# Kernel tuning notes

Hardware: AMD Instinct MI355X
Metric: run time of the kernel (lower is better)

The kernel has to match this reference:

```python
import jax, jax.numpy as jnp
import numpy as np

MRG = 0.1
ALPHA = 32.0
STAT_WEIGHT = 0.01
STAT_ADJUST_WEIGHT = 0.15
COS_EPS = 1e-8  # torch F.cosine_similarity eps


def l2_norm(x):
    # matches torch l2_norm: x / sqrt(sum(x^2, axis=1) + 1e-12)
    normp = jnp.sum(x * x, axis=1) + 1e-12
    return x / jnp.sqrt(normp)[:, None]


def setup_inputs() -> dict:
    key = jax.random.key(0)
    kx, kt, kp, kc = jax.random.split(key, 4)
    B, C, D = 512, 50000, 128
    X = jax.random.normal(kx, (B, D), dtype=jnp.float32)
    T = jax.random.randint(kt, (B,), 0, C, dtype=jnp.int32)
    proxies = jax.random.normal(kp, (C, D), dtype=jnp.float32)
    class_centers = jax.random.normal(kc, (C, D), dtype=jnp.float32)
    return {"X": X, "T": T, "proxies": proxies, "class_centers": class_centers}


def reference(X, T, proxies, class_centers):
    C = proxies.shape[0]
    Xn = l2_norm(X)                      # (B, D)
    Pn = l2_norm(proxies)                # (C, D)
    cos = Xn @ Pn.T                      # (B, C)

    # ---- vectorized per-class statistics (replaces the Python loop) ----
    counts = jax.ops.segment_sum(jnp.ones(T.shape[0], jnp.float32), T, num_segments=C)
    sums = jax.ops.segment_sum(Xn, T, num_segments=C)          # (C, D)
    sqs = jax.ops.segment_sum(Xn * Xn, T, num_segments=C)      # (C, D)
    safe = jnp.maximum(counts, 1.0)[:, None]
    mean = sums / safe
    var = jnp.clip(sqs / safe - mean * mean, 1e-6, 10.0)        # biased var, clamped
    var_weight = 1.0 / (1.0 + var.mean(axis=1))                 # (C,)

    # cosine_similarity(P_norm[i], class_centers[i]) with torch eps semantics
    pnorm = jnp.maximum(jnp.sqrt(jnp.sum(Pn * Pn, axis=1)), COS_EPS)
    cnorm = jnp.maximum(jnp.sqrt(jnp.sum(class_centers * class_centers, axis=1)), COS_EPS)
    center_sim = jnp.sum(Pn * class_centers, axis=1) / (pnorm * cnorm)  # (C,)

    has_samples = counts > 0
    adj = jnp.where(has_samples, center_sim * var_weight * STAT_ADJUST_WEIGHT, 0.0)
    combined = cos + adj[None, :]        # (B, C)

    # ---- proxy-anchor exp-sum terms ----
    onehot = (T[:, None] == jnp.arange(C, dtype=T.dtype)[None, :])  # (B, C) bool
    pos_exp = jnp.exp(-ALPHA * (combined - MRG))
    neg_exp = jnp.exp(ALPHA * (combined + MRG))
    P_sim_sum = jnp.sum(jnp.where(onehot, pos_exp, 0.0), axis=0)    # (C,)
    N_sim_sum = jnp.sum(jnp.where(onehot, 0.0, neg_exp), axis=0)    # (C,)

    num_valid = jnp.sum(has_samples).astype(jnp.float32)
    pos_term = jnp.sum(jnp.log1p(P_sim_sum)) / num_valid
    neg_term = jnp.sum(jnp.log1p(N_sim_sum)) / jnp.float32(C)

    center_reg = jnp.mean(jnp.abs(class_centers))
    return pos_term + neg_term + STAT_WEIGHT * center_reg
```

## Files before the change

### kernel.cpp

```cpp
#include <hip/hip_runtime.h>
#include <math.h>

#define ALPHA 32.0f
#define MRG 0.1f
#define STAT_WEIGHT 0.01f
#define STAT_ADJ_W 0.15f
#define COS_EPS 1e-8f

typedef __attribute__((ext_vector_type(8))) short bf16x8;
typedef __attribute__((ext_vector_type(4))) float f32x4;
typedef __attribute__((ext_vector_type(4))) unsigned int u32x4;

__device__ __forceinline__ ushort f2bf(float f) {
    unsigned u = __float_as_uint(f);
    return (ushort)((u + 0x7FFFu + ((u >> 16) & 1u)) >> 16);
}
__device__ __forceinline__ unsigned pk2(float a, float b) {
    return (unsigned)f2bf(a) | ((unsigned)f2bf(b) << 16);
}

__device__ __forceinline__ float bred128(float v, float* sm, int d) {
    #pragma unroll
    for (int off = 1; off < 64; off <<= 1) v += __shfl_xor(v, off);
    if ((d & 63) == 0) sm[d >> 6] = v;
    __syncthreads();
    float r = sm[0] + sm[1];
    __syncthreads();
    return r;
}

__global__ void k_stats(const float* __restrict__ X, const float* __restrict__ proxies,
                        const float* __restrict__ cc, const int* __restrict__ T,
                        ushort* __restrict__ Xn16, float* __restrict__ adj,
                        float* __restrict__ scal, float* __restrict__ cabs_part,
                        int C, int B) {
    const int b = blockIdx.x, d = threadIdx.x;
    __shared__ int Tl[512];
    __shared__ float sm[2];
    __shared__ float smc[2];
    __shared__ int mlist[512];
    __shared__ int mcnt;

    if (b == 0 && d < 8) scal[d] = 0.f;

    for (int i = d; i < B; i += 128) Tl[i] = T[i];
    if (d == 0) mcnt = 0;

    float cabs = 0.f;
    {
        const float4* cp = (const float4*)cc;
        const int n4 = C * 32;
        for (int i = b * 128 + d; i < n4; i += B * 128) {
            float4 v = cp[i];
            cabs += fabsf(v.x) + fabsf(v.y) + fabsf(v.z) + fabsf(v.w);
        }
    }
    #pragma unroll
    for (int off = 1; off < 64; off <<= 1) cabs += __shfl_xor(cabs, off);
    if ((d & 63) == 0) smc[d >> 6] = cabs;
    __syncthreads();
    if (d == 0) cabs_part[b] = smc[0] + smc[1];

    const int c = Tl[b];

    float x = X[(size_t)b * 128 + d];
    float n2 = bred128(x * x, sm, d);
    float xn = x * rsqrtf(n2 + 1e-12f);
    const int pk = ((((d >> 3) ^ (b & 15)) << 3) | (d & 7));
    Xn16[(size_t)b * 128 + pk] = f2bf(xn);

    for (int j = d; j < B; j += 128)
        if (Tl[j] == c) mlist[atomicAdd(&mcnt, 1)] = j;
    __syncthreads();
    const int cnt = mcnt;
    int minj = mlist[0];
    for (int i = 1; i < cnt; ++i) minj = min(minj, mlist[i]);
    if (minj != b) return;

    float sd = 0.f, qd = 0.f;
    int prev = -1;
    for (int rank = 0; rank < cnt; ++rank) {
        int cur = 0x7fffffff;
        for (int i = 0; i < cnt; ++i) { int v = mlist[i]; if (v > prev && v < cur) cur = v; }
        prev = cur;
        float xj = X[(size_t)cur * 128 + d];
        float nj = bred128(xj * xj, sm, d);
        float xnj = xj * rsqrtf(nj + 1e-12f);
        sd += xnj; qd += xnj * xnj;
    }
    float fc = (float)cnt;
    float m = sd / fc;
    float var = fminf(fmaxf(qd / fc - m * m, 1e-6f), 10.0f);
    float sv = bred128(var, sm, d);

    float p  = proxies[(size_t)c * 128 + d];
    float cv = cc[(size_t)c * 128 + d];
    float s2 = bred128(p * p, sm, d);
    float c2 = bred128(cv * cv, sm, d);
    float pc = bred128(p * cv, sm, d);
    if (d == 0) {
        float inv = rsqrtf(s2 + 1e-12f);
        float pn = fmaxf(sqrtf(s2) * inv, COS_EPS);
        float cn = fmaxf(sqrtf(c2), COS_EPS);
        float censim = (pc * inv) / (pn * cn);
        float vw = 1.0f / (1.0f + sv * (1.0f / 128.0f));
        adj[c] = censim * vw * STAT_ADJ_W;
    }
}

__launch_bounds__(256, 2)
__global__ void k_main(const float* __restrict__ proxies, const ushort* __restrict__ Xsw,
                       const int* __restrict__ T, float* __restrict__ PN,
                       int C, int nslice) {
    const int tid = threadIdx.x, lane = tid & 63, wv = tid >> 6;
    const int nlo = lane & 15, quad = lane >> 4;
    const int half = blockIdx.y;

    __shared__ ushort Sx[32768];
    __shared__ alignas(16) int Tl[256];

    {
        const uint4* src = (const uint4*)Xsw + half * 4096;
        uint4* dst = (uint4*)Sx;
        #pragma unroll
        for (int k = 0; k < 16; ++k) dst[tid + k * 256] = src[tid + k * 256];
    }
    Tl[tid] = T[half * 256 + tid];
    __syncthreads();

    float* PA = PN + (size_t)half * 2 * C;
    float* NA = PA + C;

    int fro[4];
    #pragma unroll
    for (int ks = 0; ks < 4; ++ks)
        fro[ks] = nlo * 128 + (((ks * 4 + quad) ^ nlo) << 3);

    for (int s = blockIdx.x; s < nslice; s += gridDim.x) {
        const int c0 = s * 128;
        const int cls0 = c0 + wv * 32 + nlo;
        const int cls1 = cls0 + 16;

        bf16x8 bfr[2][4];
        #pragma unroll
        for (int t = 0; t < 2; ++t) {
            int cls = c0 + wv * 32 + t * 16 + nlo;
            int cl = (cls < C) ? cls : C - 1;
            const float4* pr = (const float4*)(proxies + (size_t)cl * 128);
            float4 v0[4], v1[4];
            float s2 = 0.f;
            #pragma unroll
            for (int ks = 0; ks < 4; ++ks) {
                v0[ks] = pr[ks * 8 + quad * 2];
                v1[ks] = pr[ks * 8 + quad * 2 + 1];
                s2 += v0[ks].x*v0[ks].x + v0[ks].y*v0[ks].y + v0[ks].z*v0[ks].z + v0[ks].w*v0[ks].w
                    + v1[ks].x*v1[ks].x + v1[ks].y*v1[ks].y + v1[ks].z*v1[ks].z + v1[ks].w*v1[ks].w;
            }
            s2 += __shfl_xor(s2, 16);
            s2 += __shfl_xor(s2, 32);
            float pin = rsqrtf(s2 + 1e-12f);
            #pragma unroll
            for (int ks = 0; ks < 4; ++ks) {
                u32x4 u;
                u.x = pk2(v0[ks].x * pin, v0[ks].y * pin);
                u.y = pk2(v0[ks].z * pin, v0[ks].w * pin);
                u.z = pk2(v1[ks].x * pin, v1[ks].y * pin);
                u.w = pk2(v1[ks].z * pin, v1[ks].w * pin);
                bfr[t][ks] = __builtin_bit_cast(bf16x8, u);
            }
        }

        float pp0 = 0.f, np0 = 0.f, pp1 = 0.f, np1 = 0.f;
        #pragma unroll 4
        for (int rt = 0; rt < 16; ++rt) {
            const ushort* sb = &Sx[rt * 2048];
            bf16x8 a0 = *(const bf16x8*)&sb[fro[0]];
            bf16x8 a1 = *(const bf16x8*)&sb[fro[1]];
            bf16x8 a2 = *(const bf16x8*)&sb[fro[2]];
            bf16x8 a3 = *(const bf16x8*)&sb[fro[3]];
            f32x4 acc0 = {0.f,0.f,0.f,0.f}, acc1 = {0.f,0.f,0.f,0.f};
            acc0 = __builtin_amdgcn_mfma_f32_16x16x32_bf16(a0, bfr[0][0], acc0, 0, 0, 0);
            acc1 = __builtin_amdgcn_mfma_f32_16x16x32_bf16(a0, bfr[1][0], acc1, 0, 0, 0);
            acc0 = __builtin_amdgcn_mfma_f32_16x16x32_bf16(a1, bfr[0][1], acc0, 0, 0, 0);
            acc1 = __builtin_amdgcn_mfma_f32_16x16x32_bf16(a1, bfr[1][1], acc1, 0, 0, 0);
            acc0 = __builtin_amdgcn_mfma_f32_16x16x32_bf16(a2, bfr[0][2], acc0, 0, 0, 0);
            acc1 = __builtin_amdgcn_mfma_f32_16x16x32_bf16(a2, bfr[1][2], acc1, 0, 0, 0);
            acc0 = __builtin_amdgcn_mfma_f32_16x16x32_bf16(a3, bfr[0][3], acc0, 0, 0, 0);
            acc1 = __builtin_amdgcn_mfma_f32_16x16x32_bf16(a3, bfr[1][3], acc1, 0, 0, 0);

            int4 t4 = *(const int4*)&Tl[rt * 16 + quad * 4];
            int tvs[4] = {t4.x, t4.y, t4.z, t4.w};
            #pragma unroll
            for (int r = 0; r < 4; ++r) {
                { bool po = (tvs[r] == cls0); float v = acc0[r];
                  float e = __expf(po ? -ALPHA * (v - MRG) : ALPHA * (v + MRG));
                  pp0 += po ? e : 0.f; np0 += po ? 0.f : e; }
                { bool po = (tvs[r] == cls1); float v = acc1[r];
                  float e = __expf(po ? -ALPHA * (v - MRG) : ALPHA * (v + MRG));
                  pp1 += po ? e : 0.f; np1 += po ? 0.f : e; }
            }
        }

        pp0 += __shfl_xor(pp0, 16); pp0 += __shfl_xor(pp0, 32);
        np0 += __shfl_xor(np0, 16); np0 += __shfl_xor(np0, 32);
        pp1 += __shfl_xor(pp1, 16); pp1 += __shfl_xor(pp1, 32);
        np1 += __shfl_xor(np1, 16); np1 += __shfl_xor(np1, 32);
        if (quad == 0) {
            if (cls0 < C) { PA[cls0] = pp0; NA[cls0] = np0; }
            if (cls1 < C) { PA[cls1] = pp1; NA[cls1] = np1; }
        }
    }
}

__launch_bounds__(256)
__global__ void k_fin(const float* __restrict__ PN, const float* __restrict__ adj,
                      const float* __restrict__ cabs_part, float* __restrict__ scal,
                      float* __restrict__ out, int C, int nfin) {
    const int tid = threadIdx.x, lane = tid & 63, wv = tid >> 6;
    const int c = blockIdx.x * 256 + tid;
    __shared__ float red[4][3];
    float lp = 0.f, ln = 0.f, nv = 0.f;
    if (c < C) {
        float p = PN[c] + PN[2 * (size_t)C + c];
        float n = PN[(size_t)C + c] + PN[3 * (size_t)C + c];
        float a = 0.f;
        if (p > 0.f) { a = adj[c]; nv = 1.f; }
        lp = log1pf(p * __expf(-ALPHA * a));
        ln = log1pf(n * __expf( ALPHA * a));
    }
    #pragma unroll
    for (int off = 1; off < 64; off <<= 1) {
        lp += __shfl_xor(lp, off);
        ln += __shfl_xor(ln, off);
        nv += __shfl_xor(nv, off);
    }
    if (lane == 0) { red[wv][0] = lp; red[wv][1] = ln; red[wv][2] = nv; }
    __syncthreads();
    if (tid == 0) {
        atomicAdd(&scal[0], red[0][0] + red[1][0] + red[2][0] + red[3][0]);
        atomicAdd(&scal[1], red[0][1] + red[1][1] + red[2][1] + red[3][1]);
        atomicAdd(&scal[3], red[0][2] + red[1][2] + red[2][2] + red[3][2]);
    }
    if (blockIdx.x == 0) {
        float cb = cabs_part[tid] + cabs_part[tid + 256];
        #pragma unroll
        for (int off = 1; off < 64; off <<= 1) cb += __shfl_xor(cb, off);
        __syncthreads();
        if (lane == 0) red[wv][0] = cb;
        __syncthreads();
        if (tid == 0) atomicAdd(&scal[2], red[0][0] + red[1][0] + red[2][0] + red[3][0]);
    }
    if (tid == 0) {
        __threadfence();
        unsigned old = atomicAdd((unsigned*)(scal + 4), 1u);
        if (old == (unsigned)(nfin - 1)) {
            float S0 = atomicAdd(&scal[0], 0.f);
            float S1 = atomicAdd(&scal[1], 0.f);
            float S2 = atomicAdd(&scal[2], 0.f);
            float S3 = atomicAdd(&scal[3], 0.f);
            out[0] = S0 / S3 + S1 / (float)C + STAT_WEIGHT * (S2 / ((float)C * 128.f));
        }
    }
}

extern "C" void kernel_launch(void* const* d_in, const int* in_sizes, int n_in,
                              void* d_out, int out_size, void* d_ws, size_t ws_size,
                              hipStream_t stream) {
    const float* X       = (const float*)d_in[0];
    const int*   T       = (const int*)d_in[1];
    const float* proxies = (const float*)d_in[2];
    const float* cc      = (const float*)d_in[3];
    float* out = (float*)d_out;

    const int B = in_sizes[1];
    const int D = in_sizes[0] / B;
    const int C = in_sizes[2] / D;

    float*  PN   = (float*)d_ws;
    float*  scal = PN + 4 * (size_t)C;
    float*  cabs_part = scal + 8;
    float*  adj  = cabs_part + 512;
    ushort* Xn16 = (ushort*)(adj + C);

    const int nslice = (C + 127) / 128;
    const int nfin   = (C + 255) / 256;

    k_stats<<<B, 128, 0, stream>>>(X, proxies, cc, T, Xn16, adj, scal,
                                   cabs_part, C, B);
    k_main<<<dim3(256, 2), 256, 0, stream>>>(proxies, Xn16, T, PN, C, nslice);
    k_fin<<<nfin, 256, 0, stream>>>(PN, adj, cabs_part, scal, out, C, nfin);
}
```

Before: 130.6 us.

## Split X normalization out and co-schedule stats work with main GEMM blocks

A small prep kernel now only normalizes X into swizzled bf16. The per-class statistics and the center abs-sum move into a merged kernel, with odd blocks doing stats and even blocks doing the MFMA proxy-anchor exp-sum work. This lets the memory-heavy class_centers scan overlap with the compute-bound GEMM instead of running before it. The cost is that stats blocks also reserve the large shared-memory footprint and use 256 threads where half sit idle in the reductions. The prep kernel also keeps a dead no-op loop.

New measurement: 138.2 us. 5.8% more time.

```diff
diff --git a/kernel.cpp b/kernel.cpp
--- a/kernel.cpp
+++ b/kernel.cpp
@@ -19,57 +19,181 @@
     return (unsigned)f2bf(a) | ((unsigned)f2bf(b) << 16);
 }
 
-__device__ __forceinline__ float bred128(float v, float* sm, int d) {
+__device__ __forceinline__ float bredL(float v, float* sm, int tid) {
     #pragma unroll
     for (int off = 1; off < 64; off <<= 1) v += __shfl_xor(v, off);
-    if ((d & 63) == 0) sm[d >> 6] = v;
+    if ((tid & 63) == 0 && tid < 128) sm[tid >> 6] = v;
     __syncthreads();
     float r = sm[0] + sm[1];
     __syncthreads();
     return r;
 }
 
-__global__ void k_stats(const float* __restrict__ X, const float* __restrict__ proxies,
-                        const float* __restrict__ cc, const int* __restrict__ T,
-                        ushort* __restrict__ Xn16, float* __restrict__ adj,
-                        float* __restrict__ scal, float* __restrict__ cabs_part,
-                        int C, int B) {
+__global__ void k_prep(const float* __restrict__ X, ushort* __restrict__ Xn16,
+                       float* __restrict__ scal) {
     const int b = blockIdx.x, d = threadIdx.x;
+    __shared__ float sm[2];
+    if (b == 0 && d < 8) scal[d] = 0.f;
+    float x = X[(size_t)b * 128 + d];
+    #pragma unroll
+    for (int off = 1; off < 64; off <<= 1) x = x;
+    float v = X[(size_t)b * 128 + d];
+    float n2;
+    {
+        float s = v * v;
+        #pragma unroll
+        for (int off = 1; off < 64; off <<= 1) s += __shfl_xor(s, off);
+        if ((d & 63) == 0) sm[d >> 6] = s;
+        __syncthreads();
+        n2 = sm[0] + sm[1];
+    }
+    float xn = v * rsqrtf(n2 + 1e-12f);
+    const int pk = ((((d >> 3) ^ (b & 15)) << 3) | (d & 7));
+    Xn16[(size_t)b * 128 + pk] = f2bf(xn);
+}
+
+__launch_bounds__(256, 2)
+__global__ void k_big(const float* __restrict__ X, const float* __restrict__ proxies,
+                      const float* __restrict__ cc, const int* __restrict__ T,
+                      const ushort* __restrict__ Xsw, float* __restrict__ PN,
+                      float* __restrict__ adj, float* __restrict__ cabs_part,
+                      int C, int B, int nslice) {
+    const int tid = threadIdx.x, lane = tid & 63, wv = tid >> 6;
+    const int role = blockIdx.x & 1;
+
+    __shared__ ushort Sx[32768];
+    __shared__ alignas(16) int Tg[256];
     __shared__ int Tl[512];
+    __shared__ int mlist[512];
     __shared__ float sm[2];
-    __shared__ float smc[2];
-    __shared__ int mlist[512];
+    __shared__ float smc[8];
     __shared__ int mcnt;
 
-    if (b == 0 && d < 8) scal[d] = 0.f;
-
-    for (int i = d; i < B; i += 128) Tl[i] = T[i];
-    if (d == 0) mcnt = 0;
+    if (role == 0) {
+        const int nlo = lane & 15, quad = lane >> 4;
+        const int gid = blockIdx.x >> 1;
+        const int x = gid & 255, half = gid >> 8;
+
+        {
+            const uint4* src = (const uint4*)Xsw + half * 4096;
+            uint4* dst = (uint4*)Sx;
+            #pragma unroll
+            for (int k = 0; k < 16; ++k) dst[tid + k * 256] = src[tid + k * 256];
+        }
+        Tg[tid] = T[half * 256 + tid];
+        __syncthreads();
+
+        float* PA = PN + (size_t)half * 2 * C;
+        float* NA = PA + C;
+
+        int fro[4];
+        #pragma unroll
+        for (int ks = 0; ks < 4; ++ks)
+            fro[ks] = nlo * 128 + (((ks * 4 + quad) ^ nlo) << 3);
+
+        for (int s = x; s < nslice; s += 256) {
+            const int c0 = s * 128;
+            const int cls0 = c0 + wv * 32 + nlo;
+            const int cls1 = cls0 + 16;
+
+            bf16x8 bfr[2][4];
+            #pragma unroll
+            for (int t = 0; t < 2; ++t) {
+                int cls = c0 + wv * 32 + t * 16 + nlo;
+                int cl = (cls < C) ? cls : C - 1;
+                const float4* pr = (const float4*)(proxies + (size_t)cl * 128);
+                float4 v0[4], v1[4];
+                float s2 = 0.f;
+                #pragma unroll
+                for (int ks = 0; ks < 4; ++ks) {
+                    v0[ks] = pr[ks * 8 + quad * 2];
+                    v1[ks] = pr[ks * 8 + quad * 2 + 1];
+                    s2 += v0[ks].x*v0[ks].x + v0[ks].y*v0[ks].y + v0[ks].z*v0[ks].z + v0[ks].w*v0[ks].w
+                        + v1[ks].x*v1[ks].x + v1[ks].y*v1[ks].y + v1[ks].z*v1[ks].z + v1[ks].w*v1[ks].w;
+                }
+                s2 += __shfl_xor(s2, 16);
+                s2 += __shfl_xor(s2, 32);
+                float pin = rsqrtf(s2 + 1e-12f);
+                #pragma unroll
+                for (int ks = 0; ks < 4; ++ks) {
+                    u32x4 u;
+                    u.x = pk2(v0[ks].x * pin, v0[ks].y * pin);
+                    u.y = pk2(v0[ks].z * pin, v0[ks].w * pin);
+                    u.z = pk2(v1[ks].x * pin, v1[ks].y * pin);
+                    u.w = pk2(v1[ks].z * pin, v1[ks].w * pin);
+                    bfr[t][ks] = __builtin_bit_cast(bf16x8, u);
+                }
+            }
+
+            float pp0 = 0.f, np0 = 0.f, pp1 = 0.f, np1 = 0.f;
+            #pragma unroll 4
+            for (int rt = 0; rt < 16; ++rt) {
+                const ushort* sb = &Sx[rt * 2048];
+                bf16x8 a0 = *(const bf16x8*)&sb[fro[0]];
+                bf16x8 a1 = *(const bf16x8*)&sb[fro[1]];
+                bf16x8 a2 = *(const bf16x8*)&sb[fro[2]];
+                bf16x8 a3 = *(const bf16x8*)&sb[fro[3]];
+                f32x4 acc0 = {0.f,0.f,0.f,0.f}, acc1 = {0.f,0.f,0.f,0.f};
+                acc0 = __builtin_amdgcn_mfma_f32_16x16x32_bf16(a0, bfr[0][0], acc0, 0, 0, 0);
+                acc1 = __builtin_amdgcn_mfma_f32_16x16x32_bf16(a0, bfr[1][0], acc1, 0, 0, 0);
+                acc0 = __builtin_amdgcn_mfma_f32_16x16x32_bf16(a1, bfr[0][1], acc0, 0, 0, 0);
+                acc1 = __builtin_amdgcn_mfma_f32_16x16x32_bf16(a1, bfr[1][1], acc1, 0, 0, 0);
+                acc0 = __builtin_amdgcn_mfma_f32_16x16x32_bf16(a2, bfr[0][2], acc0, 0, 0, 0);
+                acc1 = __builtin_amdgcn_mfma_f32_16x16x32_bf16(a2, bfr[1][2], acc1, 0, 0, 0);
+                acc0 = __builtin_amdgcn_mfma_f32_16x16x32_bf16(a3, bfr[0][3], acc0, 0, 0, 0);
+                acc1 = __builtin_amdgcn_mfma_f32_16x16x32_bf16(a3, bfr[1][3], acc1, 0, 0, 0);
+
+                int4 t4 = *(const int4*)&Tg[rt * 16 + quad * 4];
+                int tvs[4] = {t4.x, t4.y, t4.z, t4.w};
+                #pragma unroll
+                for (int r = 0; r < 4; ++r) {
+                    { bool po = (tvs[r] == cls0); float v = acc0[r];
+                      float e = __expf(po ? -ALPHA * (v - MRG) : ALPHA * (v + MRG));
+                      pp0 += po ? e : 0.f; np0 += po ? 0.f : e; }
+                    { bool po = (tvs[r] == cls1); float v = acc1[r];
+                      float e = __expf(po ? -ALPHA * (v - MRG) : ALPHA * (v + MRG));
+                      pp1 += po ? e : 0.f; np1 += po ? 0.f : e; }
+                }
+            }
+
+            pp0 += __shfl_xor(pp0, 16); pp0 += __shfl_xor(pp0, 32);
+            np0 += __shfl_xor(np0, 16); np0 += __shfl_xor(np0, 32);
+            pp1 += __shfl_xor(pp1, 16); pp1 += __shfl_xor(pp1, 32);
+            np1 += __shfl_xor(np1, 16); np1 += __shfl_xor(np1, 32);
+            if (quad == 0) {
+                if (cls0 < C) { PA[cls0] = pp0; NA[cls0] = np0; }
+                if (cls1 < C) { PA[cls1] = pp1; NA[cls1] = np1; }
+            }
+        }
+        return;
+    }
+
+    const int b = blockIdx.x >> 1;
+    const int d = tid & 127;
+    const bool lo = tid < 128;
+
+    Tl[tid] = T[tid]; Tl[tid + 256] = T[tid + 256];
+    if (tid == 0) mcnt = 0;
 
     float cabs = 0.f;
     {
         const float4* cp = (const float4*)cc;
         const int n4 = C * 32;
-        for (int i = b * 128 + d; i < n4; i += B * 128) {
+        #pragma unroll 4
+        for (int i = b * 256 + tid; i < n4; i += B * 256) {
             float4 v = cp[i];
             cabs += fabsf(v.x) + fabsf(v.y) + fabsf(v.z) + fabsf(v.w);
         }
     }
     #pragma unroll
     for (int off = 1; off < 64; off <<= 1) cabs += __shfl_xor(cabs, off);
-    if ((d & 63) == 0) smc[d >> 6] = cabs;
-    __syncthreads();
-    if (d == 0) cabs_part[b] = smc[0] + smc[1];
+    if (lane == 0) smc[wv] = cabs;
+    __syncthreads();
+    if (tid == 0) cabs_part[b] = (smc[0] + smc[1]) + (smc[2] + smc[3]);
 
     const int c = Tl[b];
 
-    float x = X[(size_t)b * 128 + d];
-    float n2 = bred128(x * x, sm, d);
-    float xn = x * rsqrtf(n2 + 1e-12f);
-    const int pk = ((((d >> 3) ^ (b & 15)) << 3) | (d & 7));
-    Xn16[(size_t)b * 128 + pk] = f2bf(xn);
-
-    for (int j = d; j < B; j += 128)
+    for (int j = tid; j < B; j += 256)
         if (Tl[j] == c) mlist[atomicAdd(&mcnt, 1)] = j;
     __syncthreads();
     const int cnt = mcnt;
@@ -83,132 +207,28 @@
         int cur = 0x7fffffff;
         for (int i = 0; i < cnt; ++i) { int v = mlist[i]; if (v > prev && v < cur) cur = v; }
         prev = cur;
-        float xj = X[(size_t)cur * 128 + d];
-        float nj = bred128(xj * xj, sm, d);
+        float xj = lo ? X[(size_t)cur * 128 + d] : 0.f;
+        float nj = bredL(xj * xj, sm, tid);
         float xnj = xj * rsqrtf(nj + 1e-12f);
         sd += xnj; qd += xnj * xnj;
     }
     float fc = (float)cnt;
     float m = sd / fc;
     float var = fminf(fmaxf(qd / fc - m * m, 1e-6f), 10.0f);
-    float sv = bred128(var, sm, d);
-
-    float p  = proxies[(size_t)c * 128 + d];
-    float cv = cc[(size_t)c * 128 + d];
-    float s2 = bred128(p * p, sm, d);
-    float c2 = bred128(cv * cv, sm, d);
-    float pc = bred128(p * cv, sm, d);
-    if (d == 0) {
+    float sv = bredL(var, sm, tid);
+
+    float p  = lo ? proxies[(size_t)c * 128 + d] : 0.f;
+    float cv = lo ? cc[(size_t)c * 128 + d] : 0.f;
+    float s2 = bredL(p * p, sm, tid);
+    float c2 = bredL(cv * cv, sm, tid);
+    float pc = bredL(p * cv, sm, tid);
+    if (tid == 0) {
         float inv = rsqrtf(s2 + 1e-12f);
         float pn = fmaxf(sqrtf(s2) * inv, COS_EPS);
         float cn = fmaxf(sqrtf(c2), COS_EPS);
         float censim = (pc * inv) / (pn * cn);
         float vw = 1.0f / (1.0f + sv * (1.0f / 128.0f));
         adj[c] = censim * vw * STAT_ADJ_W;
-    }
-}
-
-__launch_bounds__(256, 2)
-__global__ void k_main(const float* __restrict__ proxies, const ushort* __restrict__ Xsw,
-                       const int* __restrict__ T, float* __restrict__ PN,
-                       int C, int nslice) {
-    const int tid = threadIdx.x, lane = tid & 63, wv = tid >> 6;
-    const int nlo = lane & 15, quad = lane >> 4;
-    const int half = blockIdx.y;
-
-    __shared__ ushort Sx[32768];
-    __shared__ alignas(16) int Tl[256];
-
-    {
-        const uint4* src = (const uint4*)Xsw + half * 4096;
-        uint4* dst = (uint4*)Sx;
-        #pragma unroll
-        for (int k = 0; k < 16; ++k) dst[tid + k * 256] = src[tid + k * 256];
-    }
-    Tl[tid] = T[half * 256 + tid];
-    __syncthreads();
-
-    float* PA = PN + (size_t)half * 2 * C;
-    float* NA = PA + C;
-
-    int fro[4];
-    #pragma unroll
-    for (int ks = 0; ks < 4; ++ks)
-        fro[ks] = nlo * 128 + (((ks * 4 + quad) ^ nlo) << 3);
-
-    for (int s = blockIdx.x; s < nslice; s += gridDim.x) {
-        const int c0 = s * 128;
-        const int cls0 = c0 + wv * 32 + nlo;
-        const int cls1 = cls0 + 16;
-
-        bf16x8 bfr[2][4];
-        #pragma unroll
-        for (int t = 0; t < 2; ++t) {
-            int cls = c0 + wv * 32 + t * 16 + nlo;
-            int cl = (cls < C) ? cls : C - 1;
-            const float4* pr = (const float4*)(proxies + (size_t)cl * 128);
-            float4 v0[4], v1[4];
-            float s2 = 0.f;
-            #pragma unroll
-            for (int ks = 0; ks < 4; ++ks) {
-                v0[ks] = pr[ks * 8 + quad * 2];
-                v1[ks] = pr[ks * 8 + quad * 2 + 1];
-                s2 += v0[ks].x*v0[ks].x + v0[ks].y*v0[ks].y + v0[ks].z*v0[ks].z + v0[ks].w*v0[ks].w
-                    + v1[ks].x*v1[ks].x + v1[ks].y*v1[ks].y + v1[ks].z*v1[ks].z + v1[ks].w*v1[ks].w;
-            }
-            s2 += __shfl_xor(s2, 16);
-            s2 += __shfl_xor(s2, 32);
-            float pin = rsqrtf(s2 + 1e-12f);
-            #pragma unroll
-            for (int ks = 0; ks < 4; ++ks) {
-                u32x4 u;
-                u.x = pk2(v0[ks].x * pin, v0[ks].y * pin);
-                u.y = pk2(v0[ks].z * pin, v0[ks].w * pin);
-                u.z = pk2(v1[ks].x * pin, v1[ks].y * pin);
-                u.w = pk2(v1[ks].z * pin, v1[ks].w * pin);
-                bfr[t][ks] = __builtin_bit_cast(bf16x8, u);
-            }
-        }
-
-        float pp0 = 0.f, np0 = 0.f, pp1 = 0.f, np1 = 0.f;
-        #pragma unroll 4
-        for (int rt = 0; rt < 16; ++rt) {
-            const ushort* sb = &Sx[rt * 2048];
-            bf16x8 a0 = *(const bf16x8*)&sb[fro[0]];
-            bf16x8 a1 = *(const bf16x8*)&sb[fro[1]];
-            bf16x8 a2 = *(const bf16x8*)&sb[fro[2]];
-            bf16x8 a3 = *(const bf16x8*)&sb[fro[3]];
-            f32x4 acc0 = {0.f,0.f,0.f,0.f}, acc1 = {0.f,0.f,0.f,0.f};
-            acc0 = __builtin_amdgcn_mfma_f32_16x16x32_bf16(a0, bfr[0][0], acc0, 0, 0, 0);
-            acc1 = __builtin_amdgcn_mfma_f32_16x16x32_bf16(a0, bfr[1][0], acc1, 0, 0, 0);
-            acc0 = __builtin_amdgcn_mfma_f32_16x16x32_bf16(a1, bfr[0][1], acc0, 0, 0, 0);
-            acc1 = __builtin_amdgcn_mfma_f32_16x16x32_bf16(a1, bfr[1][1], acc1, 0, 0, 0);
-            acc0 = __builtin_amdgcn_mfma_f32_16x16x32_bf16(a2, bfr[0][2], acc0, 0, 0, 0);
-            acc1 = __builtin_amdgcn_mfma_f32_16x16x32_bf16(a2, bfr[1][2], acc1, 0, 0, 0);
-            acc0 = __builtin_amdgcn_mfma_f32_16x16x32_bf16(a3, bfr[0][3], acc0, 0, 0, 0);
-            acc1 = __builtin_amdgcn_mfma_f32_16x16x32_bf16(a3, bfr[1][3], acc1, 0, 0, 0);
-
-            int4 t4 = *(const int4*)&Tl[rt * 16 + quad * 4];
-            int tvs[4] = {t4.x, t4.y, t4.z, t4.w};
-            #pragma unroll
-            for (int r = 0; r < 4; ++r) {
-                { bool po = (tvs[r] == cls0); float v = acc0[r];
-                  float e = __expf(po ? -ALPHA * (v - MRG) : ALPHA * (v + MRG));
-                  pp0 += po ? e : 0.f; np0 += po ? 0.f : e; }
-                { bool po = (tvs[r] == cls1); float v = acc1[r];
-                  float e = __expf(po ? -ALPHA * (v - MRG) : ALPHA * (v + MRG));
-                  pp1 += po ? e : 0.f; np1 += po ? 0.f : e; }
-            }
-        }
-
-        pp0 += __shfl_xor(pp0, 16); pp0 += __shfl_xor(pp0, 32);
-        np0 += __shfl_xor(np0, 16); np0 += __shfl_xor(np0, 32);
-        pp1 += __shfl_xor(pp1, 16); pp1 += __shfl_xor(pp1, 32);
-        np1 += __shfl_xor(np1, 16); np1 += __shfl_xor(np1, 32);
-        if (quad == 0) {
-            if (cls0 < C) { PA[cls0] = pp0; NA[cls0] = np0; }
-            if (cls1 < C) { PA[cls1] = pp1; NA[cls1] = np1; }
-        }
     }
 }
 
@@ -285,8 +305,8 @@
     const int nslice = (C + 127) / 128;
     const int nfin   = (C + 255) / 256;
 
-    k_stats<<<B, 128, 0, stream>>>(X, proxies, cc, T, Xn16, adj, scal,
-                                   cabs_part, C, B);
-    k_main<<<dim3(256, 2), 256, 0, stream>>>(proxies, Xn16, T, PN, C, nslice);
+    k_prep<<<B, 128, 0, stream>>>(X, Xn16, scal);
+    k_big<<<1024, 256, 0, stream>>>(X, proxies, cc, T, Xn16, PN, adj,
+                                    cabs_part, C, B, nslice);
     k_fin<<<nfin, 256, 0, stream>>>(PN, adj, cabs_part, scal, out, C, nfin);
 }
```
